# Kernel optimization log

Hardware: AMD Instinct MI355X
Metric: run time of the kernel (lower is better)

## Reference

```python
import jax, jax.numpy as jnp
import numpy as np

H = 256
W = 256
CHUNK = 100  # faces per rasterizer scan step


def _cross2(o, p, q):
    # 2D cross product of (p-o) x (q-o); broadcasts over leading dims
    return (p[..., 0] - o[..., 0]) * (q[..., 1] - o[..., 1]) - (p[..., 1] - o[..., 1]) * (q[..., 0] - o[..., 0])


def transform(verts, K, Rt):
    # verts [B,V,3] -> pixel coords [B,V,3] = (x_pix, y_pix, z_cam)
    v_cam = jnp.einsum('bij,bnj->bni', Rt[:, :, :3], verts) + Rt[:, None, :, 3]
    v_proj = jnp.einsum('bij,bnj->bni', K, v_cam)
    z = v_cam[..., 2:3]
    return jnp.concatenate([v_proj[..., :2] / z, z], axis=-1)


def _pixel_centers(h, w, dtype):
    px = jnp.arange(w, dtype=dtype) + 0.5
    py = jnp.arange(h, dtype=dtype) + 0.5
    gx, gy = jnp.meshgrid(px, py, indexing='xy')  # [h,w]
    return gx, gy


def rasterize(v_pix, vi, h, w):
    # z-buffered triangle rasterization -> index image [B,h,w] (int32, -1 = bg)
    B = v_pix.shape[0]
    Fc = vi.shape[0]
    gx, gy = _pixel_centers(h, w, v_pix.dtype)
    pix = jnp.stack([gx.ravel(), gy.ravel()], axis=-1)  # [HW,2]
    face_ids = jnp.arange(Fc, dtype=jnp.int32).reshape(-1, CHUNK)
    inf = jnp.asarray(jnp.inf, v_pix.dtype)

    def step(carry, fids):
        best_z, best_i = carry
        tri = vi[fids]                      # [C,3]
        p = v_pix[:, tri]                   # [B,C,3,3]
        a, b, c = p[:, :, 0], p[:, :, 1], p[:, :, 2]
        area = _cross2(a[..., :2], b[..., :2], c[..., :2])  # [B,C]
        pixb = pix[None, None]              # [1,1,HW,2]
        w0 = _cross2(b[..., None, :2], c[..., None, :2], pixb)  # [B,C,HW]
        w1 = _cross2(c[..., None, :2], a[..., None, :2], pixb)
        w2 = _cross2(a[..., None, :2], b[..., None, :2], pixb)
        s = jnp.sign(area)[..., None]
        nz = jnp.abs(area)[..., None] > 1e-8
        inside = (w0 * s >= 0) & (w1 * s >= 0) & (w2 * s >= 0) & nz
        za, zb, zc = a[..., 2:3], b[..., 2:3], c[..., 2:3]
        valid = inside & (za > 0) & (zb > 0) & (zc > 0)
        ar = jnp.where(jnp.abs(area) > 1e-8, area, 1.0)[..., None]
        invz = (w0 / ar) / za + (w1 / ar) / zb + (w2 / ar) / zc  # persp-correct 1/z
        z = jnp.where(valid & (invz > 0), 1.0 / jnp.maximum(invz, 1e-12), inf)
        cz = z.min(axis=1)                  # [B,HW]
        ci = z.argmin(axis=1)
        cf = fids[ci]
        upd = cz < best_z
        return (jnp.where(upd, cz, best_z), jnp.where(upd, cf, best_i)), None

    init = (jnp.full((B, h * w), jnp.inf, v_pix.dtype), jnp.full((B, h * w), -1, jnp.int32))
    (_, bi), _ = jax.lax.scan(step, init, face_ids)
    return bi.reshape(B, h, w)


def render(v_pix, vi, index_img):
    # depth [B,h,w] and perspective-correct barycentrics [B,3,h,w]
    B, h, w = index_img.shape
    tri = vi[jnp.clip(index_img, 0)]                 # [B,h,w,3]
    p = jax.vmap(lambda v, t: v[t])(v_pix, tri)      # [B,h,w,3,3]
    gx, gy = _pixel_centers(h, w, v_pix.dtype)
    pt = jnp.stack([gx, gy], axis=-1)[None]          # [1,h,w,2]
    a, b, c = p[..., 0, :], p[..., 1, :], p[..., 2, :]
    w0 = _cross2(b[..., :2], c[..., :2], pt)
    w1 = _cross2(c[..., :2], a[..., :2], pt)
    w2 = _cross2(a[..., :2], b[..., :2], pt)
    area = w0 + w1 + w2
    ar = jnp.where(jnp.abs(area) > 1e-8, area, 1.0)
    f0 = (w0 / ar) / jnp.maximum(a[..., 2], 1e-8)
    f1 = (w1 / ar) / jnp.maximum(b[..., 2], 1e-8)
    f2 = (w2 / ar) / jnp.maximum(c[..., 2], 1e-8)
    invz = f0 + f1 + f2
    invz_s = jnp.where(jnp.abs(invz) > 1e-12, invz, 1.0)
    depth = 1.0 / invz_s
    bary = jnp.stack([f0, f1, f2], axis=-1) / invz_s[..., None]  # [B,h,w,3]
    m = index_img != -1
    depth_img = jnp.where(m, depth, 0.0)
    bary_img = jnp.where(m[..., None], bary, 0.0).transpose(0, 3, 1, 2)  # [B,3,h,w]
    return depth_img, bary_img


def interpolate(attr, vti, index_img, bary_img):
    # attr [B,N,D], bary_img [B,3,h,w] -> [B,D,h,w]
    tri = vti[jnp.clip(index_img, 0)]                # [B,h,w,3]
    av = jax.vmap(lambda a, t: a[t])(attr, tri)      # [B,h,w,3,D]
    return jnp.einsum('bhwkd,bkhw->bdhw', av, bary_img)


def grid_sample_bilinear(tex, grid):
    # tex [B,C,Ht,Wt], grid [B,h,w,2] in [-1,1]; align_corners=False, zero pad
    B, C, Ht, Wt = tex.shape
    x = (grid[..., 0] + 1.0) * Wt / 2.0 - 0.5
    y = (grid[..., 1] + 1.0) * Ht / 2.0 - 0.5
    x0 = jnp.floor(x)
    y0 = jnp.floor(y)
    wx = (x - x0)[:, None]
    wy = (y - y0)[:, None]
    x0i = x0.astype(jnp.int32)
    y0i = y0.astype(jnp.int32)

    def gat(ix, iy):
        valid = (ix >= 0) & (ix < Wt) & (iy >= 0) & (iy < Ht)
        ixc = jnp.clip(ix, 0, Wt - 1)
        iyc = jnp.clip(iy, 0, Ht - 1)
        v = jax.vmap(lambda t, yy, xx: t[:, yy, xx])(tex, iyc, ixc)  # [B,C,h,w]
        return v * valid[:, None].astype(tex.dtype)

    return (gat(x0i, y0i) * (1 - wx) * (1 - wy)
            + gat(x0i + 1, y0i) * wx * (1 - wy)
            + gat(x0i, y0i + 1) * (1 - wx) * wy
            + gat(x0i + 1, y0i + 1) * wx * wy)


def reference(verts, tex, K, Rt, vt, vi, vti):
    v_pix = transform(verts, K, Rt)
    index_img = jax.lax.stop_gradient(rasterize(v_pix, vi, H, W))
    depth_img, bary_img = render(v_pix, vi, index_img)
    B = verts.shape[0]
    vt_attr = jnp.broadcast_to((vt * 2.0 - 1.0)[None], (B,) + vt.shape)
    vt_img = interpolate(vt_attr, vti, index_img, bary_img)    # [B,2,H,W]
    mask = (index_img != -1)[:, None].astype(tex.dtype)
    img = grid_sample_bilinear(tex, vt_img.transpose(0, 2, 3, 1)) * mask
    # edge_grad_estimator is identity in the forward pass
    return img, depth_img, v_pix, vt_img, index_img, bary_img, mask


def setup_inputs() -> dict:
    key = jax.random.key(0)
    ks = jax.random.split(key, 6)
    B, V, Fc, Nvt = 2, 5000, 10000, 5000
    xy = jax.random.uniform(ks[0], (B, V, 2), minval=-1.5, maxval=1.5)
    z = jax.random.uniform(ks[1], (B, V, 1), minval=2.0, maxval=4.0)
    verts = jnp.concatenate([xy, z], axis=-1)
    tex = jax.random.uniform(ks[2], (B, 3, 1024, 1024), dtype=jnp.float32)
    K = jnp.broadcast_to(jnp.array([[256., 0., 128.], [0., 256., 128.], [0., 0., 1.]], dtype=jnp.float32), (B, 3, 3))
    Rt = jnp.broadcast_to(jnp.concatenate([jnp.eye(3, dtype=jnp.float32), jnp.zeros((3, 1), jnp.float32)], axis=1), (B, 3, 4))
    vt = jax.random.uniform(ks[3], (Nvt, 2), dtype=jnp.float32)
    vi = jax.random.randint(ks[4], (Fc, 3), 0, V).astype(jnp.int32)
    vti = jax.random.randint(ks[5], (Fc, 3), 0, Nvt).astype(jnp.int32)
    return {"verts": verts, "tex": tex, "K": K, "Rt": Rt, "vt": vt, "vi": vi, "vti": vti}
```

## Files before the change

### kernel.cpp

```cpp
#include <hip/hip_runtime.h>
#include <cmath>

#define H_ 256
#define W_ 256
#define SEG 4
#define NB 256
#define REC_STRIDE 24
#define INITKEY 0x7f800000FFFFFFFFull

__device__ inline unsigned fkey(float f) {
  unsigned u = __float_as_uint(f);
  return (u & 0x80000000u) ? ~u : (u | 0x80000000u);
}
__device__ inline float unfkey(unsigned k) {
  return (k & 0x80000000u) ? __uint_as_float(k & 0x7fffffffu) : __uint_as_float(~k);
}

__global__ void k_transform(const float* __restrict__ verts, const float* __restrict__ Km,
                            const float* __restrict__ Rt, float* __restrict__ vpix,
                            int B, int V) {
  int i = blockIdx.x * blockDim.x + threadIdx.x;
  if (i >= B * V) return;
  int b = i / V;
  float x = verts[(size_t)i * 3 + 0], y = verts[(size_t)i * 3 + 1], z = verts[(size_t)i * 3 + 2];
  const float* R = Rt + (size_t)b * 12;
  float cx = __fadd_rn(__fadd_rn(__fadd_rn(__fmul_rn(R[0], x), __fmul_rn(R[1], y)), __fmul_rn(R[2], z)), R[3]);
  float cy = __fadd_rn(__fadd_rn(__fadd_rn(__fmul_rn(R[4], x), __fmul_rn(R[5], y)), __fmul_rn(R[6], z)), R[7]);
  float cz = __fadd_rn(__fadd_rn(__fadd_rn(__fmul_rn(R[8], x), __fmul_rn(R[9], y)), __fmul_rn(R[10], z)), R[11]);
  const float* Kb = Km + (size_t)b * 9;
  float px = __fadd_rn(__fadd_rn(__fmul_rn(Kb[0], cx), __fmul_rn(Kb[1], cy)), __fmul_rn(Kb[2], cz));
  float py = __fadd_rn(__fadd_rn(__fmul_rn(Kb[3], cx), __fmul_rn(Kb[4], cy)), __fmul_rn(Kb[5], cz));
  vpix[(size_t)i * 3 + 0] = __fdiv_rn(px, cz);
  vpix[(size_t)i * 3 + 1] = __fdiv_rn(py, cz);
  vpix[(size_t)i * 3 + 2] = cz;
}

__global__ void k_init(unsigned long long* __restrict__ keys, int nkeys,
                       int* __restrict__ hist, int* __restrict__ cursor, int nbkt,
                       unsigned* __restrict__ minmax) {
  int i = blockIdx.x * blockDim.x + threadIdx.x;
  if (keys && i < nkeys) keys[i] = INITKEY;
  if (i < nbkt) { hist[i] = 0; cursor[i] = 0; }
  if (i == 0 && minmax) { minmax[0] = 0xFFFFFFFFu; minmax[1] = 0u; }
}

__global__ void k_faceprep(const float* __restrict__ vpix, const int* __restrict__ vi,
                           float* __restrict__ rec, unsigned* __restrict__ minmax,
                           int B, int V, int F) {
  int i = blockIdx.x * blockDim.x + threadIdx.x;
  if (i >= B * F) return;
  int b = i / F, f = i - b * F;
  int i0 = vi[f * 3 + 0], i1 = vi[f * 3 + 1], i2 = vi[f * 3 + 2];
  const float* base = vpix + (size_t)b * V * 3;
  float ax = base[(size_t)i0 * 3], ay = base[(size_t)i0 * 3 + 1], az = base[(size_t)i0 * 3 + 2];
  float bx = base[(size_t)i1 * 3], by = base[(size_t)i1 * 3 + 1], bz = base[(size_t)i1 * 3 + 2];
  float cx = base[(size_t)i2 * 3], cy = base[(size_t)i2 * 3 + 1], cz = base[(size_t)i2 * 3 + 2];
  float e0x = __fsub_rn(cx, bx), e0y = __fsub_rn(cy, by);
  float e1x = __fsub_rn(ax, cx), e1y = __fsub_rn(ay, cy);
  float e2x = __fsub_rn(bx, ax), e2y = __fsub_rn(by, ay);
  float area = __fsub_rn(__fmul_rn(e2x, __fsub_rn(cy, ay)), __fmul_rn(e2y, __fsub_rn(cx, ax)));
  float s = (area > 0.f) ? 1.f : ((area < 0.f) ? -1.f : 0.f);
  bool nz = fabsf(area) > 1e-8f;
  bool zv = (az > 0.f) && (bz > 0.f) && (cz > 0.f);
  float sprime = (nz && zv) ? s : __uint_as_float(0x7fc00000u);
  float ar = nz ? area : 1.0f;
  float zmin = fminf(az, fminf(bz, cz));
  float* r = rec + (size_t)i * REC_STRIDE;
  r[0] = ax; r[1] = ay; r[2] = bx; r[3] = by; r[4] = cx; r[5] = cy;
  r[6] = e0x; r[7] = e0y; r[8] = e1x; r[9] = e1y; r[10] = e2x; r[11] = e2y;
  r[12] = az; r[13] = bz; r[14] = cz; r[15] = sprime; r[16] = ar;
  r[17] = fminf(ax, fminf(bx, cx));
  r[18] = fmaxf(ax, fmaxf(bx, cx));
  r[19] = fminf(ay, fminf(by, cy));
  r[20] = fmaxf(ay, fmaxf(by, cy));
  r[21] = zmin; r[22] = 0.f; r[23] = 0.f;
  if (minmax && zmin == zmin) {
    unsigned k = fkey(zmin);
    atomicMin(&minmax[0], k);
    atomicMax(&minmax[1], k);
  }
}

__global__ void k_hist(const float* __restrict__ rec, const unsigned* __restrict__ minmax,
                       int* __restrict__ hist, int B, int F) {
  int i = blockIdx.x * blockDim.x + threadIdx.x;
  if (i >= B * F) return;
  int b = i / F;
  float zmin = rec[(size_t)i * REC_STRIDE + 21];
  float zlo = unfkey(minmax[0]), zhi = unfkey(minmax[1]);
  float scale = (float)NB / fmaxf(zhi - zlo, 1e-12f);
  int bkt = 0;
  if (zmin == zmin) bkt = min(NB - 1, max(0, (int)((zmin - zlo) * scale)));
  atomicAdd(&hist[b * NB + bkt], 1);
}

__global__ void k_scan(const int* __restrict__ hist, int* __restrict__ boff, int B) {
  __shared__ int sh[NB];
  int t = threadIdx.x;
  for (int b = 0; b < B; ++b) {
    sh[t] = hist[b * NB + t];
    __syncthreads();
    int self = sh[t];
    for (int ofs = 1; ofs < NB; ofs <<= 1) {
      int u = (t >= ofs) ? sh[t - ofs] : 0;
      __syncthreads();
      sh[t] += u;
      __syncthreads();
    }
    boff[b * NB + t] = sh[t] - self;
    __syncthreads();
  }
}

__global__ void k_scatter(const float* __restrict__ rec, const unsigned* __restrict__ minmax,
                          const int* __restrict__ boff, int* __restrict__ cursor,
                          float4* __restrict__ srec, float4* __restrict__ sbb,
                          float* __restrict__ szf, int B, int F) {
  int i = blockIdx.x * blockDim.x + threadIdx.x;
  if (i >= B * F) return;
  int b = i / F, f = i - b * F;
  const float* r = rec + (size_t)i * REC_STRIDE;
  float zmin = r[21];
  float zlo = unfkey(minmax[0]), zhi = unfkey(minmax[1]);
  float rng = fmaxf(zhi - zlo, 1e-12f);
  float scale = (float)NB / rng;
  int bkt = 0;
  if (zmin == zmin) bkt = min(NB - 1, max(0, (int)((zmin - zlo) * scale)));
  float floorval = zlo + (float)bkt * (rng / (float)NB);
  int pos = boff[b * NB + bkt] + atomicAdd(&cursor[b * NB + bkt], 1);
  size_t gp = (size_t)b * F + pos;
  szf[gp] = floorval;
  sbb[gp] = make_float4(r[17], r[18], r[19], r[20]);
  float4* d = srec + gp * 5;
  d[0] = make_float4(r[0], r[1], r[2], r[3]);
  d[1] = make_float4(r[4], r[5], r[6], r[7]);
  d[2] = make_float4(r[8], r[9], r[10], r[11]);
  d[3] = make_float4(r[12], r[13], r[14], r[15]);
  d[4] = make_float4(r[16], r[21], __int_as_float(f), 0.f);
}

__global__ __launch_bounds__(256) void k_raster_tile(const float4* __restrict__ srec,
                                                     const float4* __restrict__ sbb,
                                                     const float* __restrict__ szf,
                                                     float* __restrict__ o_idx,
                                                     int B, int F) {
  int seg = blockIdx.x;
  int y   = blockIdx.y;
  int b   = blockIdx.z;
  int tid = threadIdx.x;
  int w = tid >> 6, lane = tid & 63;
  __shared__ unsigned long long sk[64];
  if (tid < 64) sk[tid] = INITKEY;
  __syncthreads();
  const float4* srb  = srec + (size_t)b * F * 5;
  const float4* sbbb = sbb + (size_t)b * F;
  const float*  szfb = szf + (size_t)b * F;
  float px = seg * 64 + lane + 0.5f, py = y + 0.5f;
  float wx0 = seg * 64 + 0.5f, wx1 = wx0 + 63.0f;
  unsigned long long bestkey = INITKEY;
  float bestz = INFINITY;
  int it = 0;
  int pos = w;
  float zfl = (pos < F) ? szfb[pos] : 0.f;
  float4 bb = (pos < F) ? sbbb[pos] : make_float4(0.f, 0.f, 0.f, 0.f);
  for (; pos < F; pos += 4, ++it) {
    int nxt = pos + 4;
    float zfl_n = 0.f;
    float4 bb_n = bb;
    if (nxt < F) { zfl_n = szfb[nxt]; bb_n = sbbb[nxt]; }
    float floor0 = __fmul_rn(zfl, 0.9999f) - 1e-5f;
    if (__all(floor0 > bestz)) break;
    if ((it & 7) == 7) {
      unsigned long long old = atomicMin(&sk[lane], bestkey);
      if (old < bestkey) { bestkey = old; bestz = __uint_as_float((unsigned)(bestkey >> 32)); }
    }
    bool cull = (py < bb.z) || (py > bb.w) || (bb.y < wx0) || (bb.x > wx1);
    if (!cull) {
      float4 r0 = srb[(size_t)pos * 5 + 0];
      float4 r1 = srb[(size_t)pos * 5 + 1];
      float4 r2 = srb[(size_t)pos * 5 + 2];
      float4 r3 = srb[(size_t)pos * 5 + 3];
      float4 r4 = srb[(size_t)pos * 5 + 4];
      float w0 = __fsub_rn(__fmul_rn(r1.z, __fsub_rn(py, r0.w)), __fmul_rn(r1.w, __fsub_rn(px, r0.z)));
      float w1 = __fsub_rn(__fmul_rn(r2.x, __fsub_rn(py, r1.y)), __fmul_rn(r2.y, __fsub_rn(px, r1.x)));
      float w2 = __fsub_rn(__fmul_rn(r2.z, __fsub_rn(py, r0.y)), __fmul_rn(r2.w, __fsub_rn(px, r0.x)));
      float sp = r3.w;
      bool inside = (__fmul_rn(w0, sp) >= 0.f) && (__fmul_rn(w1, sp) >= 0.f) && (__fmul_rn(w2, sp) >= 0.f);
      if (inside && !(__fmul_rn(r4.y, 0.9999f) > bestz)) {
        float t0 = __fdiv_rn(__fdiv_rn(w0, r4.x), r3.x);
        float t1 = __fdiv_rn(__fdiv_rn(w1, r4.x), r3.y);
        float t2 = __fdiv_rn(__fdiv_rn(w2, r4.x), r3.z);
        float invz = __fadd_rn(__fadd_rn(t0, t1), t2);
        if (invz > 0.f) {
          float z = __fdiv_rn(1.0f, fmaxf(invz, 1e-12f));
          int fid = __float_as_int(r4.z);
          unsigned long long ck = ((unsigned long long)__float_as_uint(z) << 32) | (unsigned)fid;
          if (ck < bestkey) {
            bestkey = ck;
            bestz = __uint_as_float((unsigned)(bestkey >> 32));
            atomicMin(&sk[lane], ck);
          }
        }
      }
    }
    zfl = zfl_n; bb = bb_n;
  }
  atomicMin(&sk[lane], bestkey);
  __syncthreads();
  if (tid < 64) {
    unsigned long long k = sk[tid];
    unsigned zb = (unsigned)(k >> 32);
    o_idx[(size_t)b * (H_ * W_) + (size_t)y * W_ + seg * 64 + tid] =
        (zb >= 0x7f800000u) ? -1.0f : (float)(int)(unsigned)(k & 0xffffffffu);
  }
}

__global__ __launch_bounds__(256) void k_raster(const float* __restrict__ rec,
                                                unsigned long long* __restrict__ keys,
                                                int B, int F) {
  int x = threadIdx.x;
  int y = blockIdx.x;
  int b = blockIdx.y;
  int seg = blockIdx.z;
  int f0 = (int)((long long)seg * F / SEG);
  int f1 = (int)((long long)(seg + 1) * F / SEG);
  float px = x + 0.5f, py = y + 0.5f;
  float bestz = INFINITY; int besti = -1;
  const float* rb = rec + (size_t)b * F * REC_STRIDE;
  for (int f = f0; f < f1; ++f) {
    const float* r = rb + (size_t)f * REC_STRIDE;
    float miny = r[19], maxy = r[20], minx = r[17], maxx = r[18];
    if (py < miny || py > maxy || maxx < 0.5f || minx > (float)W_ - 0.5f) continue;
    float e0x = r[6], e0y = r[7], e1x = r[8], e1y = r[9], e2x = r[10], e2y = r[11];
    float za = r[12], zb = r[13], zc = r[14], sp = r[15], ar = r[16];
    float w0 = __fsub_rn(__fmul_rn(e0x, __fsub_rn(py, r[3])), __fmul_rn(e0y, __fsub_rn(px, r[2])));
    float w1 = __fsub_rn(__fmul_rn(e1x, __fsub_rn(py, r[5])), __fmul_rn(e1y, __fsub_rn(px, r[4])));
    float w2 = __fsub_rn(__fmul_rn(e2x, __fsub_rn(py, r[1])), __fmul_rn(e2y, __fsub_rn(px, r[0])));
    bool inside = (__fmul_rn(w0, sp) >= 0.f) && (__fmul_rn(w1, sp) >= 0.f) && (__fmul_rn(w2, sp) >= 0.f);
    if (inside) {
      float t0 = __fdiv_rn(__fdiv_rn(w0, ar), za);
      float t1 = __fdiv_rn(__fdiv_rn(w1, ar), zb);
      float t2 = __fdiv_rn(__fdiv_rn(w2, ar), zc);
      float invz = __fadd_rn(__fadd_rn(t0, t1), t2);
      if (invz > 0.f) {
        float z = __fdiv_rn(1.0f, fmaxf(invz, 1e-12f));
        if (z < bestz) { bestz = z; besti = f; }
      }
    }
  }
  if (besti >= 0) {
    unsigned long long key = ((unsigned long long)__float_as_uint(bestz) << 32) | (unsigned)besti;
    atomicMin(&keys[(size_t)b * (H_ * W_) + y * W_ + x], key);
  }
}

__global__ void k_resolve(const unsigned long long* __restrict__ keys, float* __restrict__ idxout, int n) {
  int i = blockIdx.x * blockDim.x + threadIdx.x;
  if (i >= n) return;
  unsigned long long k = keys[i];
  unsigned zb = (unsigned)(k >> 32);
  idxout[i] = (zb >= 0x7f800000u) ? -1.0f : (float)(int)(unsigned)(k & 0xffffffffu);
}

__global__ void k_raster_direct(const float* __restrict__ vpix, const int* __restrict__ vi,
                                float* __restrict__ idxout, int B, int V, int F) {
  int p = blockIdx.x * blockDim.x + threadIdx.x;
  if (p >= B * H_ * W_) return;
  int b = p / (H_ * W_); int pid = p - b * (H_ * W_);
  float px = (pid & (W_ - 1)) + 0.5f, py = (pid >> 8) + 0.5f;
  const float* base = vpix + (size_t)b * V * 3;
  float bestz = INFINITY; int besti = -1;
  for (int f = 0; f < F; ++f) {
    int i0 = vi[f * 3], i1 = vi[f * 3 + 1], i2 = vi[f * 3 + 2];
    float ax = base[(size_t)i0 * 3], ay = base[(size_t)i0 * 3 + 1], za = base[(size_t)i0 * 3 + 2];
    float bx = base[(size_t)i1 * 3], by = base[(size_t)i1 * 3 + 1], zb = base[(size_t)i1 * 3 + 2];
    float cx = base[(size_t)i2 * 3], cy = base[(size_t)i2 * 3 + 1], zc = base[(size_t)i2 * 3 + 2];
    float e0x = __fsub_rn(cx, bx), e0y = __fsub_rn(cy, by);
    float e1x = __fsub_rn(ax, cx), e1y = __fsub_rn(ay, cy);
    float e2x = __fsub_rn(bx, ax), e2y = __fsub_rn(by, ay);
    float area = __fsub_rn(__fmul_rn(e2x, __fsub_rn(cy, ay)), __fmul_rn(e2y, __fsub_rn(cx, ax)));
    float s = (area > 0.f) ? 1.f : ((area < 0.f) ? -1.f : 0.f);
    bool nz = fabsf(area) > 1e-8f;
    bool zv = (za > 0.f) && (zb > 0.f) && (zc > 0.f);
    float sp = (nz && zv) ? s : __uint_as_float(0x7fc00000u);
    float ar = nz ? area : 1.0f;
    float w0 = __fsub_rn(__fmul_rn(e0x, __fsub_rn(py, by)), __fmul_rn(e0y, __fsub_rn(px, bx)));
    float w1 = __fsub_rn(__fmul_rn(e1x, __fsub_rn(py, cy)), __fmul_rn(e1y, __fsub_rn(px, cx)));
    float w2 = __fsub_rn(__fmul_rn(e2x, __fsub_rn(py, ay)), __fmul_rn(e2y, __fsub_rn(px, ax)));
    bool inside = (__fmul_rn(w0, sp) >= 0.f) && (__fmul_rn(w1, sp) >= 0.f) && (__fmul_rn(w2, sp) >= 0.f);
    if (inside) {
      float invz = __fadd_rn(__fadd_rn(__fdiv_rn(__fdiv_rn(w0, ar), za),
                                       __fdiv_rn(__fdiv_rn(w1, ar), zb)),
                             __fdiv_rn(__fdiv_rn(w2, ar), zc));
      if (invz > 0.f) {
        float z = __fdiv_rn(1.0f, fmaxf(invz, 1e-12f));
        if (z < bestz) { bestz = z; besti = f; }
      }
    }
  }
  idxout[p] = (float)besti;
}

__global__ __launch_bounds__(256) void k_render(const float* __restrict__ vpix, const int* __restrict__ vi,
                                                const int* __restrict__ vti, const float* __restrict__ vt,
                                                const float* __restrict__ tex, const float* __restrict__ idxin,
                                                float* __restrict__ o_img, float* __restrict__ o_depth,
                                                float* __restrict__ o_vt, float* __restrict__ o_bary,
                                                float* __restrict__ o_mask,
                                                int B, int V, int F, int TH, int TW) {
  int p = blockIdx.x * blockDim.x + threadIdx.x;
  if (p >= B * H_ * W_) return;
  int HW = H_ * W_;
  int b = p / HW; int pid = p - b * HW;
  int y = pid >> 8, x = pid & (W_ - 1);
  int idx = (int)idxin[p];
  size_t pix2 = (size_t)b * 2 * HW + pid;
  size_t pix3 = (size_t)b * 3 * HW + pid;
  if (idx < 0) {
    o_depth[p] = 0.f; o_mask[p] = 0.f;
    o_vt[pix2] = 0.f; o_vt[pix2 + HW] = 0.f;
    o_bary[pix3] = 0.f; o_bary[pix3 + HW] = 0.f; o_bary[pix3 + 2 * HW] = 0.f;
    o_img[pix3] = 0.f; o_img[pix3 + HW] = 0.f; o_img[pix3 + 2 * HW] = 0.f;
    return;
  }
  const float* base = vpix + (size_t)b * V * 3;
  int i0 = vi[idx * 3], i1 = vi[idx * 3 + 1], i2 = vi[idx * 3 + 2];
  float ax = base[(size_t)i0 * 3], ay = base[(size_t)i0 * 3 + 1], az = base[(size_t)i0 * 3 + 2];
  float bx = base[(size_t)i1 * 3], by = base[(size_t)i1 * 3 + 1], bz = base[(size_t)i1 * 3 + 2];
  float cx = base[(size_t)i2 * 3], cy = base[(size_t)i2 * 3 + 1], cz = base[(size_t)i2 * 3 + 2];
  float ptx = x + 0.5f, pty = y + 0.5f;
  float w0 = __fsub_rn(__fmul_rn(__fsub_rn(cx, bx), __fsub_rn(pty, by)),
                       __fmul_rn(__fsub_rn(cy, by), __fsub_rn(ptx, bx)));
  float w1 = __fsub_rn(__fmul_rn(__fsub_rn(ax, cx), __fsub_rn(pty, cy)),
                       __fmul_rn(__fsub_rn(ay, cy), __fsub_rn(ptx, cx)));
  float w2 = __fsub_rn(__fmul_rn(__fsub_rn(bx, ax), __fsub_rn(pty, ay)),
                       __fmul_rn(__fsub_rn(by, ay), __fsub_rn(ptx, ax)));
  float area = __fadd_rn(__fadd_rn(w0, w1), w2);
  float ar = (fabsf(area) > 1e-8f) ? area : 1.0f;
  float f0 = __fdiv_rn(__fdiv_rn(w0, ar), fmaxf(az, 1e-8f));
  float f1 = __fdiv_rn(__fdiv_rn(w1, ar), fmaxf(bz, 1e-8f));
  float f2 = __fdiv_rn(__fdiv_rn(w2, ar), fmaxf(cz, 1e-8f));
  float invz = __fadd_rn(__fadd_rn(f0, f1), f2);
  float invz_s = (fabsf(invz) > 1e-12f) ? invz : 1.0f;
  float depth = __fdiv_rn(1.0f, invz_s);
  float bary0 = __fdiv_rn(f0, invz_s);
  float bary1 = __fdiv_rn(f1, invz_s);
  float bary2 = __fdiv_rn(f2, invz_s);
  o_depth[p] = depth; o_mask[p] = 1.0f;
  o_bary[pix3] = bary0; o_bary[pix3 + HW] = bary1; o_bary[pix3 + 2 * HW] = bary2;
  int t0 = vti[idx * 3], t1 = vti[idx * 3 + 1], t2 = vti[idx * 3 + 2];
  float u0x = __fsub_rn(__fmul_rn(vt[(size_t)t0 * 2], 2.f), 1.f);
  float u0y = __fsub_rn(__fmul_rn(vt[(size_t)t0 * 2 + 1], 2.f), 1.f);
  float u1x = __fsub_rn(__fmul_rn(vt[(size_t)t1 * 2], 2.f), 1.f);
  float u1y = __fsub_rn(__fmul_rn(vt[(size_t)t1 * 2 + 1], 2.f), 1.f);
  float u2x = __fsub_rn(__fmul_rn(vt[(size_t)t2 * 2], 2.f), 1.f);
  float u2y = __fsub_rn(__fmul_rn(vt[(size_t)t2 * 2 + 1], 2.f), 1.f);
  float gx = __fadd_rn(__fadd_rn(__fmul_rn(u0x, bary0), __fmul_rn(u1x, bary1)), __fmul_rn(u2x, bary2));
  float gy = __fadd_rn(__fadd_rn(__fmul_rn(u0y, bary0), __fmul_rn(u1y, bary1)), __fmul_rn(u2y, bary2));
  o_vt[pix2] = gx; o_vt[pix2 + HW] = gy;
  float sx = __fsub_rn(__fdiv_rn(__fmul_rn(__fadd_rn(gx, 1.0f), (float)TW), 2.0f), 0.5f);
  float sy = __fsub_rn(__fdiv_rn(__fmul_rn(__fadd_rn(gy, 1.0f), (float)TH), 2.0f), 0.5f);
  float x0f = floorf(sx), y0f = floorf(sy);
  float wx = __fsub_rn(sx, x0f), wy = __fsub_rn(sy, y0f);
  float omx = __fsub_rn(1.0f, wx), omy = __fsub_rn(1.0f, wy);
  int x0 = (int)x0f, y0 = (int)y0f;
  int x1 = x0 + 1, y1 = y0 + 1;
  bool v00 = (x0 >= 0) && (x0 < TW) && (y0 >= 0) && (y0 < TH);
  bool v10 = (x1 >= 0) && (x1 < TW) && (y0 >= 0) && (y0 < TH);
  bool v01 = (x0 >= 0) && (x0 < TW) && (y1 >= 0) && (y1 < TH);
  bool v11 = (x1 >= 0) && (x1 < TW) && (y1 >= 0) && (y1 < TH);
  int x0c = min(max(x0, 0), TW - 1), x1c = min(max(x1, 0), TW - 1);
  int y0c = min(max(y0, 0), TH - 1), y1c = min(max(y1, 0), TH - 1);
  const float* tb = tex + (size_t)b * 3 * TH * TW;
  #pragma unroll
  for (int ch = 0; ch < 3; ++ch) {
    const float* tc = tb + (size_t)ch * TH * TW;
    float g00 = v00 ? tc[(size_t)y0c * TW + x0c] : 0.f;
    float g10 = v10 ? tc[(size_t)y0c * TW + x1c] : 0.f;
    float g01 = v01 ? tc[(size_t)y1c * TW + x0c] : 0.f;
    float g11 = v11 ? tc[(size_t)y1c * TW + x1c] : 0.f;
    float r = __fmul_rn(__fmul_rn(g00, omx), omy);
    r = __fadd_rn(r, __fmul_rn(__fmul_rn(g10, wx), omy));
    r = __fadd_rn(r, __fmul_rn(__fmul_rn(g01, omx), wy));
    r = __fadd_rn(r, __fmul_rn(__fmul_rn(g11, wx), wy));
    o_img[pix3 + (size_t)ch * HW] = r;
  }
}

extern "C" void kernel_launch(void* const* d_in, const int* in_sizes, int n_in,
                              void* d_out, int out_size, void* d_ws, size_t ws_size,
                              hipStream_t stream) {
  const float* verts = (const float*)d_in[0];
  const float* tex   = (const float*)d_in[1];
  const float* Km    = (const float*)d_in[2];
  const float* Rt    = (const float*)d_in[3];
  const float* vt    = (const float*)d_in[4];
  const int*   vi    = (const int*)d_in[5];
  const int*   vti   = (const int*)d_in[6];

  int B = in_sizes[2] / 9;
  int V = in_sizes[0] / (3 * B);
  int F = in_sizes[5] / 3;
  long texhw = (long)in_sizes[1] / (B * 3);
  int TH = (int)(sqrt((double)texhw) + 0.5);
  int TW = TH;
  const int HW = H_ * W_;

  float* out = (float*)d_out;
  float* o_img   = out;
  float* o_depth = o_img + (size_t)B * 3 * HW;
  float* o_vpix  = o_depth + (size_t)B * HW;
  float* o_vt    = o_vpix + (size_t)B * V * 3;
  float* o_idx   = o_vt + (size_t)B * 2 * HW;
  float* o_bary  = o_idx + (size_t)B * HW;
  float* o_mask  = o_bary + (size_t)B * 3 * HW;

  k_transform<<<(B * V + 255) / 256, 256, 0, stream>>>(verts, Km, Rt, o_vpix, B, V);

  size_t srecBytes   = (size_t)B * F * 5 * 16;
  size_t sbbBytes    = (size_t)B * F * 16;
  size_t recBytes    = (size_t)B * F * REC_STRIDE * 4;
  size_t szfBytes    = (size_t)B * F * 4;
  size_t histBytes   = (size_t)B * NB * 4;
  size_t keysBytes   = (size_t)B * HW * 8;
  size_t needSorted = srecBytes + sbbBytes + recBytes + szfBytes + 3 * histBytes + 16;
  size_t needBasic  = keysBytes + recBytes;

  if (ws_size >= needSorted) {
    char* w = (char*)d_ws;
    float4* srec = (float4*)w;                                    w += srecBytes;
    float4* sbb  = (float4*)w;                                    w += sbbBytes;
    float*  rec  = (float*)w;                                     w += recBytes;
    float*  szf  = (float*)w;                                     w += szfBytes;
    int*    hist = (int*)w;                                       w += histBytes;
    int*    boff = (int*)w;                                       w += histBytes;
    int*    cursor = (int*)w;                                     w += histBytes;
    unsigned* minmax = (unsigned*)w;

    k_init<<<(B * NB + 255) / 256, 256, 0, stream>>>((unsigned long long*)nullptr, 0, hist, cursor, B * NB, minmax);
    k_faceprep<<<(B * F + 255) / 256, 256, 0, stream>>>(o_vpix, vi, rec, minmax, B, V, F);
    k_hist<<<(B * F + 255) / 256, 256, 0, stream>>>(rec, minmax, hist, B, F);
    k_scan<<<1, NB, 0, stream>>>(hist, boff, B);
    k_scatter<<<(B * F + 255) / 256, 256, 0, stream>>>(rec, minmax, boff, cursor, srec, sbb, szf, B, F);
    dim3 rg(W_ / 64, H_, B);
    k_raster_tile<<<rg, 256, 0, stream>>>(srec, sbb, szf, o_idx, B, F);
  } else if (ws_size >= needBasic) {
    unsigned long long* keys = (unsigned long long*)d_ws;
    float* rec = (float*)((char*)d_ws + keysBytes);
    k_init<<<(B * HW + 255) / 256, 256, 0, stream>>>(keys, B * HW, (int*)nullptr, (int*)nullptr, 0, (unsigned*)nullptr);
    k_faceprep<<<(B * F + 255) / 256, 256, 0, stream>>>(o_vpix, vi, rec, (unsigned*)nullptr, B, V, F);
    dim3 rg(H_, B, SEG);
    k_raster<<<rg, 256, 0, stream>>>(rec, keys, B, F);
    k_resolve<<<(B * HW + 255) / 256, 256, 0, stream>>>(keys, o_idx, B * HW);
  } else {
    k_raster_direct<<<(B * HW + 255) / 256, 256, 0, stream>>>(o_vpix, vi, o_idx, B, V, F);
  }

  k_render<<<(B * HW + 255) / 256, 256, 0, stream>>>(o_vpix, vi, vti, vt, tex, o_idx,
                                                     o_img, o_depth, o_vt, o_bary, o_mask,
                                                     B, V, F, TH, TW);
}
```

Before: 405.8 us.

## Split sorted face records into SoA arrays and use bucket-based early termination

The scatter now writes face data as separate float4 arrays, with the sign pre-multiplied into the edge coefficients. This removes the per-edge sign multiplies, and z and face id are loaded only for covered pixels. The raster kernel grows from 4 to 8 waves per block. The per-iteration depth-floor load and wave-wide break are replaced by a periodic reduction of the worst best-z across the row segment, which maps to a depth bucket and shrinks the loop limit to that bucket's start offset. The fmul-rounded sign premultiplication and the new cutoff arithmetic risk small numerical divergence. The larger blocks may reduce occupancy.

Result: slower. 454.0 us (+11.9%).

```diff
diff --git a/kernel.cpp b/kernel.cpp
--- a/kernel.cpp
+++ b/kernel.cpp
@@ -5,6 +5,7 @@
 #define W_ 256
 #define SEG 4
 #define NB 256
+#define ILV 8
 #define REC_STRIDE 24
 #define INITKEY 0x7f800000FFFFFFFFull
 
@@ -114,8 +115,10 @@
 
 __global__ void k_scatter(const float* __restrict__ rec, const unsigned* __restrict__ minmax,
                           const int* __restrict__ boff, int* __restrict__ cursor,
-                          float4* __restrict__ srec, float4* __restrict__ sbb,
-                          float* __restrict__ szf, int B, int F) {
+                          float4* __restrict__ sA, float4* __restrict__ sB4,
+                          float4* __restrict__ sC, float4* __restrict__ sZ,
+                          float4* __restrict__ sbb, int* __restrict__ sfid,
+                          int B, int F) {
   int i = blockIdx.x * blockDim.x + threadIdx.x;
   if (i >= B * F) return;
   int b = i / F, f = i - b * F;
@@ -126,84 +129,93 @@
   float scale = (float)NB / rng;
   int bkt = 0;
   if (zmin == zmin) bkt = min(NB - 1, max(0, (int)((zmin - zlo) * scale)));
-  float floorval = zlo + (float)bkt * (rng / (float)NB);
   int pos = boff[b * NB + bkt] + atomicAdd(&cursor[b * NB + bkt], 1);
   size_t gp = (size_t)b * F + pos;
-  szf[gp] = floorval;
+  float sp = r[15];
   sbb[gp] = make_float4(r[17], r[18], r[19], r[20]);
-  float4* d = srec + gp * 5;
-  d[0] = make_float4(r[0], r[1], r[2], r[3]);
-  d[1] = make_float4(r[4], r[5], r[6], r[7]);
-  d[2] = make_float4(r[8], r[9], r[10], r[11]);
-  d[3] = make_float4(r[12], r[13], r[14], r[15]);
-  d[4] = make_float4(r[16], r[21], __int_as_float(f), 0.f);
-}
-
-__global__ __launch_bounds__(256) void k_raster_tile(const float4* __restrict__ srec,
-                                                     const float4* __restrict__ sbb,
-                                                     const float* __restrict__ szf,
-                                                     float* __restrict__ o_idx,
-                                                     int B, int F) {
+  sA[gp]  = make_float4(r[0], r[1], r[2], r[3]);
+  sB4[gp] = make_float4(r[4], r[5], __fmul_rn(sp, r[6]), __fmul_rn(sp, r[7]));
+  sC[gp]  = make_float4(__fmul_rn(sp, r[8]), __fmul_rn(sp, r[9]),
+                        __fmul_rn(sp, r[10]), __fmul_rn(sp, r[11]));
+  sZ[gp]  = make_float4(r[12], r[13], r[14], __fmul_rn(sp, r[16]));
+  sfid[gp] = f;
+}
+
+__global__ __launch_bounds__(64 * ILV) void k_raster_tile(const float4* __restrict__ sA,
+                                                          const float4* __restrict__ sB4,
+                                                          const float4* __restrict__ sC,
+                                                          const float4* __restrict__ sZ,
+                                                          const float4* __restrict__ sbb,
+                                                          const int* __restrict__ sfid,
+                                                          const int* __restrict__ boff,
+                                                          const unsigned* __restrict__ minmax,
+                                                          float* __restrict__ o_idx,
+                                                          int B, int F) {
   int seg = blockIdx.x;
   int y   = blockIdx.y;
   int b   = blockIdx.z;
   int tid = threadIdx.x;
   int w = tid >> 6, lane = tid & 63;
   __shared__ unsigned long long sk[64];
+  __shared__ int bstart[NB + 1];
   if (tid < 64) sk[tid] = INITKEY;
+  if (tid < NB) bstart[tid] = boff[b * NB + tid];
+  if (tid == 0) bstart[NB] = F;
   __syncthreads();
-  const float4* srb  = srec + (size_t)b * F * 5;
-  const float4* sbbb = sbb + (size_t)b * F;
-  const float*  szfb = szf + (size_t)b * F;
+  float zlo = unfkey(minmax[0]), zhi = unfkey(minmax[1]);
+  float rng = fmaxf(zhi - zlo, 1e-12f);
+  float stepv = __fdiv_rn(rng, (float)NB);
+  size_t fb = (size_t)b * F;
   float px = seg * 64 + lane + 0.5f, py = y + 0.5f;
   float wx0 = seg * 64 + 0.5f, wx1 = wx0 + 63.0f;
   unsigned long long bestkey = INITKEY;
-  float bestz = INFINITY;
+  int limit = F;
   int it = 0;
-  int pos = w;
-  float zfl = (pos < F) ? szfb[pos] : 0.f;
-  float4 bb = (pos < F) ? sbbb[pos] : make_float4(0.f, 0.f, 0.f, 0.f);
-  for (; pos < F; pos += 4, ++it) {
-    int nxt = pos + 4;
-    float zfl_n = 0.f;
-    float4 bb_n = bb;
-    if (nxt < F) { zfl_n = szfb[nxt]; bb_n = sbbb[nxt]; }
-    float floor0 = __fmul_rn(zfl, 0.9999f) - 1e-5f;
-    if (__all(floor0 > bestz)) break;
-    if ((it & 7) == 7) {
-      unsigned long long old = atomicMin(&sk[lane], bestkey);
-      if (old < bestkey) { bestkey = old; bestz = __uint_as_float((unsigned)(bestkey >> 32)); }
-    }
+  for (int pos = w; pos < limit; pos += ILV) {
+    float4 bb = sbb[fb + pos];
     bool cull = (py < bb.z) || (py > bb.w) || (bb.y < wx0) || (bb.x > wx1);
     if (!cull) {
-      float4 r0 = srb[(size_t)pos * 5 + 0];
-      float4 r1 = srb[(size_t)pos * 5 + 1];
-      float4 r2 = srb[(size_t)pos * 5 + 2];
-      float4 r3 = srb[(size_t)pos * 5 + 3];
-      float4 r4 = srb[(size_t)pos * 5 + 4];
-      float w0 = __fsub_rn(__fmul_rn(r1.z, __fsub_rn(py, r0.w)), __fmul_rn(r1.w, __fsub_rn(px, r0.z)));
-      float w1 = __fsub_rn(__fmul_rn(r2.x, __fsub_rn(py, r1.y)), __fmul_rn(r2.y, __fsub_rn(px, r1.x)));
-      float w2 = __fsub_rn(__fmul_rn(r2.z, __fsub_rn(py, r0.y)), __fmul_rn(r2.w, __fsub_rn(px, r0.x)));
-      float sp = r3.w;
-      bool inside = (__fmul_rn(w0, sp) >= 0.f) && (__fmul_rn(w1, sp) >= 0.f) && (__fmul_rn(w2, sp) >= 0.f);
-      if (inside && !(__fmul_rn(r4.y, 0.9999f) > bestz)) {
-        float t0 = __fdiv_rn(__fdiv_rn(w0, r4.x), r3.x);
-        float t1 = __fdiv_rn(__fdiv_rn(w1, r4.x), r3.y);
-        float t2 = __fdiv_rn(__fdiv_rn(w2, r4.x), r3.z);
-        float invz = __fadd_rn(__fadd_rn(t0, t1), t2);
+      float4 a0 = sA[fb + pos];
+      float4 a1 = sB4[fb + pos];
+      float4 a2 = sC[fb + pos];
+      float t0 = __fsub_rn(__fmul_rn(a1.z, __fsub_rn(py, a0.w)), __fmul_rn(a1.w, __fsub_rn(px, a0.z)));
+      float t1 = __fsub_rn(__fmul_rn(a2.x, __fsub_rn(py, a1.y)), __fmul_rn(a2.y, __fsub_rn(px, a1.x)));
+      float t2 = __fsub_rn(__fmul_rn(a2.z, __fsub_rn(py, a0.y)), __fmul_rn(a2.w, __fsub_rn(px, a0.x)));
+      bool inside = (t0 >= 0.f) && (t1 >= 0.f) && (t2 >= 0.f);
+      if (inside) {
+        float4 zz = sZ[fb + pos];
+        float u0 = __fdiv_rn(__fdiv_rn(t0, zz.w), zz.x);
+        float u1 = __fdiv_rn(__fdiv_rn(t1, zz.w), zz.y);
+        float u2 = __fdiv_rn(__fdiv_rn(t2, zz.w), zz.z);
+        float invz = __fadd_rn(__fadd_rn(u0, u1), u2);
         if (invz > 0.f) {
           float z = __fdiv_rn(1.0f, fmaxf(invz, 1e-12f));
-          int fid = __float_as_int(r4.z);
+          int fid = sfid[fb + pos];
           unsigned long long ck = ((unsigned long long)__float_as_uint(z) << 32) | (unsigned)fid;
           if (ck < bestkey) {
             bestkey = ck;
-            bestz = __uint_as_float((unsigned)(bestkey >> 32));
             atomicMin(&sk[lane], ck);
           }
         }
       }
     }
-    zfl = zfl_n; bb = bb_n;
+    ++it;
+    if ((it & 7) == 0) {
+      unsigned long long old = atomicMin(&sk[lane], bestkey);
+      if (old < bestkey) bestkey = old;
+      float bz = __uint_as_float((unsigned)(bestkey >> 32));
+      #pragma unroll
+      for (int m = 32; m >= 1; m >>= 1) bz = fmaxf(bz, __shfl_xor(bz, m));
+      if (bz < 3.0e38f) {
+        float q = __fdiv_rn(__fsub_rn(__fdiv_rn(__fadd_rn(bz, 1e-5f), 0.9999f), zlo), stepv);
+        int k = (int)floorf(q) - 2;
+        if (k < 0) k = 0;
+        while (k < NB &&
+               !(__fsub_rn(__fmul_rn(__fadd_rn(zlo, __fmul_rn((float)k, stepv)), 0.9999f), 1e-5f) > bz))
+          ++k;
+        limit = bstart[k];
+      }
+    }
   }
   atomicMin(&sk[lane], bestkey);
   __syncthreads();
@@ -417,33 +429,36 @@
 
   k_transform<<<(B * V + 255) / 256, 256, 0, stream>>>(verts, Km, Rt, o_vpix, B, V);
 
-  size_t srecBytes   = (size_t)B * F * 5 * 16;
-  size_t sbbBytes    = (size_t)B * F * 16;
-  size_t recBytes    = (size_t)B * F * REC_STRIDE * 4;
-  size_t szfBytes    = (size_t)B * F * 4;
-  size_t histBytes   = (size_t)B * NB * 4;
-  size_t keysBytes   = (size_t)B * HW * 8;
-  size_t needSorted = srecBytes + sbbBytes + recBytes + szfBytes + 3 * histBytes + 16;
+  size_t f4Bytes   = (size_t)B * F * 16;
+  size_t recBytes  = (size_t)B * F * REC_STRIDE * 4;
+  size_t fidBytes  = (size_t)B * F * 4;
+  size_t histBytes = (size_t)B * NB * 4;
+  size_t keysBytes = (size_t)B * HW * 8;
+  size_t needSorted = 5 * f4Bytes + recBytes + fidBytes + 3 * histBytes + 16;
   size_t needBasic  = keysBytes + recBytes;
 
   if (ws_size >= needSorted) {
     char* w = (char*)d_ws;
-    float4* srec = (float4*)w;                                    w += srecBytes;
-    float4* sbb  = (float4*)w;                                    w += sbbBytes;
-    float*  rec  = (float*)w;                                     w += recBytes;
-    float*  szf  = (float*)w;                                     w += szfBytes;
-    int*    hist = (int*)w;                                       w += histBytes;
-    int*    boff = (int*)w;                                       w += histBytes;
-    int*    cursor = (int*)w;                                     w += histBytes;
+    float4* sA  = (float4*)w;  w += f4Bytes;
+    float4* sB4 = (float4*)w;  w += f4Bytes;
+    float4* sC  = (float4*)w;  w += f4Bytes;
+    float4* sZ  = (float4*)w;  w += f4Bytes;
+    float4* sbb = (float4*)w;  w += f4Bytes;
+    float*  rec = (float*)w;   w += recBytes;
+    int*    sfid = (int*)w;    w += fidBytes;
+    int*    hist = (int*)w;    w += histBytes;
+    int*    boff = (int*)w;    w += histBytes;
+    int*    cursor = (int*)w;  w += histBytes;
     unsigned* minmax = (unsigned*)w;
 
     k_init<<<(B * NB + 255) / 256, 256, 0, stream>>>((unsigned long long*)nullptr, 0, hist, cursor, B * NB, minmax);
     k_faceprep<<<(B * F + 255) / 256, 256, 0, stream>>>(o_vpix, vi, rec, minmax, B, V, F);
     k_hist<<<(B * F + 255) / 256, 256, 0, stream>>>(rec, minmax, hist, B, F);
     k_scan<<<1, NB, 0, stream>>>(hist, boff, B);
-    k_scatter<<<(B * F + 255) / 256, 256, 0, stream>>>(rec, minmax, boff, cursor, srec, sbb, szf, B, F);
+    k_scatter<<<(B * F + 255) / 256, 256, 0, stream>>>(rec, minmax, boff, cursor,
+                                                       sA, sB4, sC, sZ, sbb, sfid, B, F);
     dim3 rg(W_ / 64, H_, B);
-    k_raster_tile<<<rg, 256, 0, stream>>>(srec, sbb, szf, o_idx, B, F);
+    k_raster_tile<<<rg, 64 * ILV, 0, stream>>>(sA, sB4, sC, sZ, sbb, sfid, boff, minmax, o_idx, B, F);
   } else if (ws_size >= needBasic) {
     unsigned long long* keys = (unsigned long long*)d_ws;
     float* rec = (float*)((char*)d_ws + keysBytes);
```
